# Optimization experiments

Hardware: AMD Instinct MI355X
Metric: run time of the kernel (lower is better)

## Reference

```python
import jax, jax.numpy as jnp
import numpy as np
import math

N_HEAD = 16
HEAD_DIM = 64
N_EMBD = 1024
EPS_RMS = 1e-5
U_L2_EPS = 1e-6

def _get_alibi_slopes(n_heads):
    def pow2(n):
        start = 2 ** (-2 ** (-(math.log2(n) - 3)))
        return [start * start ** i for i in range(n)]
    if math.log2(n_heads).is_integer():
        return pow2(n_heads)
    c = 2 ** math.floor(math.log2(n_heads))
    s = pow2(c)
    extra = _get_alibi_slopes(2 * c)
    return s + extra[0::2][: n_heads - c]

def setup_inputs() -> dict:
    key = jax.random.key(0)
    ks = jax.random.split(key, 9)
    B, T = 2, 2048
    H, D, C = N_HEAD, HEAD_DIM, N_EMBD
    x = jax.random.normal(ks[0], (B, T, C), dtype=jnp.float32)
    # Linear weights stored as [in, out] so y = x @ W
    sc = 1.0 / math.sqrt(C)
    Wq = jax.random.normal(ks[1], (C, H * D), dtype=jnp.float32) * sc
    Wk = jax.random.normal(ks[2], (C, H * D), dtype=jnp.float32) * sc
    Wv = jax.random.normal(ks[3], (C, H * D), dtype=jnp.float32) * sc
    Wproj = jax.random.normal(ks[4], (H * D, C), dtype=jnp.float32) * (0.5 / math.sqrt(C) / math.sqrt(12))
    q_rms_w = jnp.ones((D,), dtype=jnp.float32)
    k_rms_w = jnp.ones((D,), dtype=jnp.float32)
    # keygated bias params: omega init = softplus_inverse(1.0), u ~ N(0, 1/sqrt(D))
    omega = jnp.full((H,), math.log(math.expm1(1.0)), dtype=jnp.float32)
    u = jax.random.normal(ks[5], (H, D), dtype=jnp.float32) * (1.0 / math.sqrt(D))
    return {"x": x, "Wq": Wq, "Wk": Wk, "Wv": Wv, "Wproj": Wproj,
            "q_rms_w": q_rms_w, "k_rms_w": k_rms_w, "omega": omega, "u": u}

def _rmsnorm(x, w):
    var = jnp.mean(jnp.square(x), axis=-1, keepdims=True)
    return x * jax.lax.rsqrt(var + EPS_RMS) * w

def reference(x, Wq, Wk, Wv, Wproj, q_rms_w, k_rms_w, omega, u):
    B, T, C = x.shape
    H, D = N_HEAD, HEAD_DIM
    q = (x @ Wq).reshape(B, T, H, D)
    k = (x @ Wk).reshape(B, T, H, D)
    v = (x @ Wv).reshape(B, T, H, D)
    q = _rmsnorm(q, q_rms_w)
    k = _rmsnorm(k, k_rms_w)
    # key-gated additive bias
    slopes = jnp.asarray(_get_alibi_slopes(H), dtype=jnp.float32)  # [H]
    omega_eff = jax.nn.softplus(omega) * slopes                    # [H]
    u_n = u / jnp.maximum(jnp.linalg.norm(u, axis=-1, keepdims=True), U_L2_EPS)
    gate_logits = jnp.einsum('bthd,hd->bht', k, u_n) / math.sqrt(D)  # fp32
    gate = jax.nn.softplus(gate_logits)                            # [B,H,T]
    idx = jnp.arange(T)
    dist = jnp.maximum(idx[:, None] - idx[None, :], 0).astype(jnp.float32)  # [T,T]
    bias = -dist[None, None] * omega_eff[None, :, None, None] * gate[:, :, None, :]  # [B,H,T,T]
    causal = idx[:, None] >= idx[None, :]
    bias = jnp.where(causal[None, None], bias, -jnp.inf)
    # attention
    scale = 1.0 / math.sqrt(D)
    scores = jnp.einsum('bihd,bjhd->bhij', q, k) * scale + bias
    attn = jax.nn.softmax(scores, axis=-1)
    y = jnp.einsum('bhij,bjhd->bihd', attn, v).reshape(B, T, H * D)
    return y @ Wproj
```

## Files before the change

kernel.cpp:

```cpp
#include <hip/hip_runtime.h>
#include <hip/hip_bf16.h>

#define NH 16
#define HD 64
#define CE 1024
#define TT 2048
#define BB 2
#define MR (BB*TT)

typedef __attribute__((ext_vector_type(4))) float f32x4;
typedef __attribute__((ext_vector_type(8))) short s16x8;

__device__ __forceinline__ unsigned short f2b(float f) {
  union { __hip_bfloat16 b; unsigned short u; } t;
  t.b = __float2bfloat16(f);
  return t.u;
}
__device__ __forceinline__ float red64_sum(float v) {
#pragma unroll
  for (int m = 1; m < 64; m <<= 1) v += __shfl_xor(v, m, 64);
  return v;
}
__device__ __forceinline__ float red16_sum(float v) {
#pragma unroll
  for (int m = 1; m < 16; m <<= 1) v += __shfl_xor(v, m, 64);
  return v;
}
__device__ __forceinline__ float red16_max(float v) {
#pragma unroll
  for (int m = 1; m < 16; m <<= 1) v = fmaxf(v, __shfl_xor(v, m, 64));
  return v;
}
__device__ __forceinline__ float softplusf(float x) {
  return x > 20.0f ? x : log1pf(expf(x));
}

__global__ __launch_bounds__(256) void cvt_x(const float* __restrict__ x,
                                             unsigned short* __restrict__ xb, int n4) {
  int stride = gridDim.x * blockDim.x;
  for (int i = blockIdx.x * blockDim.x + threadIdx.x; i < n4; i += stride) {
    float4 v = ((const float4*)x)[i];
    union { unsigned short u[4]; uint2 p; } o;
    o.u[0] = f2b(v.x); o.u[1] = f2b(v.y); o.u[2] = f2b(v.z); o.u[3] = f2b(v.w);
    ((uint2*)xb)[i] = o.p;
  }
}

__global__ __launch_bounds__(256) void cvt_wt(const float* __restrict__ W0, const float* __restrict__ W1,
                                              const float* __restrict__ W2, const float* __restrict__ W3,
                                              unsigned short* __restrict__ T0, unsigned short* __restrict__ T1,
                                              unsigned short* __restrict__ T2, unsigned short* __restrict__ T3) {
  const float* W = blockIdx.z == 0 ? W0 : blockIdx.z == 1 ? W1 : blockIdx.z == 2 ? W2 : W3;
  unsigned short* T = blockIdx.z == 0 ? T0 : blockIdx.z == 1 ? T1 : blockIdx.z == 2 ? T2 : T3;
  __shared__ float t[64][65];
  int k0 = blockIdx.x * 64, n0 = blockIdx.y * 64;
  int row = threadIdx.x >> 2, seg = threadIdx.x & 3;
#pragma unroll
  for (int i = 0; i < 4; ++i) {
    float4 v = *(const float4*)(W + (size_t)(k0 + row) * CE + n0 + seg * 16 + i * 4);
    int c = seg * 16 + i * 4;
    t[row][c + 0] = v.x; t[row][c + 1] = v.y; t[row][c + 2] = v.z; t[row][c + 3] = v.w;
  }
  __syncthreads();
#pragma unroll
  for (int it = 0; it < 2; ++it) {
    int c = threadIdx.x + it * 256;
    int n = c >> 3, ks = (c & 7) * 8;
    union { unsigned short u[8]; uint4 p; } o;
#pragma unroll
    for (int e = 0; e < 8; ++e) o.u[e] = f2b(t[ks + e][n]);
    *(uint4*)(T + (size_t)(n0 + n) * CE + k0 + ks) = o.p;
  }
}

#define BM 128
#define BN 128
#define BK 64
__global__ __launch_bounds__(256) void gemm3(const unsigned short* __restrict__ A,
    const unsigned short* __restrict__ B0, const unsigned short* __restrict__ B1,
    const unsigned short* __restrict__ B2,
    float* __restrict__ C0, float* __restrict__ C1, float* __restrict__ C2,
    int M, int N, int K) {
  const unsigned short* Bt = blockIdx.z == 0 ? B0 : blockIdx.z == 1 ? B1 : B2;
  float* C = blockIdx.z == 0 ? C0 : blockIdx.z == 1 ? C1 : C2;
  __shared__ __align__(16) unsigned short aT[BM * BK];
  __shared__ __align__(16) unsigned short bT[BN * BK];
  int tid = threadIdx.x;
  int w = tid >> 6, lane = tid & 63, q4 = lane >> 4, r16 = lane & 15;
  int m0 = blockIdx.y * BM, n0 = blockIdx.x * BN;
  int wm = (w >> 1) * 64, wn = (w & 1) * 64;
  f32x4 acc[4][4] = {};
  for (int k0 = 0; k0 < K; k0 += BK) {
#pragma unroll
    for (int it = 0; it < 4; ++it) {
      int c = tid + it * 256;
      int row = c >> 3, sl = c & 7;
      s16x8 va = *(const s16x8*)(A + (size_t)(m0 + row) * K + k0 + sl * 8);
      *(s16x8*)((char*)aT + row * 128 + ((sl ^ (row & 7)) << 4)) = va;
      s16x8 vb = *(const s16x8*)(Bt + (size_t)(n0 + row) * K + k0 + sl * 8);
      *(s16x8*)((char*)bT + row * 128 + ((sl ^ (row & 7)) << 4)) = vb;
    }
    __syncthreads();
#pragma unroll
    for (int kk = 0; kk < 2; ++kk) {
      s16x8 af[4], bfr[4];
#pragma unroll
      for (int i = 0; i < 4; ++i) {
        int ra = wm + i * 16 + r16;
        af[i] = *(const s16x8*)((char*)aT + ra * 128 + ((((kk << 2) | q4) ^ (ra & 7)) << 4));
        int rb = wn + i * 16 + r16;
        bfr[i] = *(const s16x8*)((char*)bT + rb * 128 + ((((kk << 2) | q4) ^ (rb & 7)) << 4));
      }
#pragma unroll
      for (int i = 0; i < 4; ++i)
#pragma unroll
        for (int j = 0; j < 4; ++j)
          acc[i][j] = __builtin_amdgcn_mfma_f32_16x16x32_bf16(af[i], bfr[j], acc[i][j], 0, 0, 0);
    }
    __syncthreads();
  }
#pragma unroll
  for (int i = 0; i < 4; ++i)
#pragma unroll
    for (int j = 0; j < 4; ++j)
#pragma unroll
      for (int r = 0; r < 4; ++r) {
        int gm = m0 + wm + i * 16 + (q4 << 2) + r;
        int gn = n0 + wn + j * 16 + r16;
        C[(size_t)gm * N + gn] = acc[i][j][r];
      }
}

__global__ __launch_bounds__(256) void rmsgate(const float* __restrict__ q, const float* __restrict__ k,
    const float* __restrict__ v, const float* __restrict__ qw, const float* __restrict__ kw,
    const float* __restrict__ omega, const float* __restrict__ u,
    unsigned short* __restrict__ qb, unsigned short* __restrict__ kb,
    unsigned short* __restrict__ vtb, float* __restrict__ cg) {
  int b = blockIdx.z, h = blockIdx.y, t0 = blockIdx.x * 64;
  int tid = threadIdx.x, w = tid >> 6, lane = tid & 63;
  float uv = u[h * HD + lane];
  float us = red64_sum(uv * uv);
  float un = uv / fmaxf(sqrtf(us), 1e-6f);
  float qwl = qw[lane], kwl = kw[lane];
  float weff = softplusf(omega[h]) * exp2f(-0.5f * (float)(h + 1));
  size_t hb = ((size_t)(b * NH + h)) * TT;
#pragma unroll 4
  for (int it = 0; it < 16; ++it) {
    int t = t0 + w * 16 + it;
    size_t roff = ((size_t)(b * TT + t)) * CE + h * HD + lane;
    float qv = q[roff];
    float rq = rsqrtf(red64_sum(qv * qv) * (1.0f / 64.0f) + 1e-5f);
    qb[(hb + t) * HD + lane] = f2b(qv * rq * qwl * 0.125f);
    float kv = k[roff];
    float rk = rsqrtf(red64_sum(kv * kv) * (1.0f / 64.0f) + 1e-5f);
    float kn = kv * rk * kwl;
    kb[(hb + t) * HD + lane] = f2b(kn);
    float gl = red64_sum(kn * un) * 0.125f;
    if (lane == 0) cg[hb + t] = weff * softplusf(gl);
  }
  __shared__ unsigned short vt[64 * 65];
  int row = tid >> 2, seg = tid & 3;
#pragma unroll
  for (int i = 0; i < 4; ++i) {
    float4 vv = *(const float4*)(v + ((size_t)(b * TT + t0 + row)) * CE + h * HD + seg * 16 + i * 4);
    int d = seg * 16 + i * 4;
    vt[(d + 0) * 65 + row] = f2b(vv.x);
    vt[(d + 1) * 65 + row] = f2b(vv.y);
    vt[(d + 2) * 65 + row] = f2b(vv.z);
    vt[(d + 3) * 65 + row] = f2b(vv.w);
  }
  __syncthreads();
#pragma unroll
  for (int it = 0; it < 2; ++it) {
    int c = tid + it * 256;
    int d = c >> 3, js = (c & 7) * 8;
    union { unsigned short u[8]; uint4 p; } o;
#pragma unroll
    for (int e = 0; e < 8; ++e) o.u[e] = vt[d * 65 + js + e];
    *(uint4*)(vtb + (((size_t)(b * NH + h)) * HD + d) * TT + t0 + js) = o.p;
  }
}

#define QB 64
#define KVB 64
__global__ __launch_bounds__(256) void attn(const unsigned short* __restrict__ qb,
    const unsigned short* __restrict__ kb, const unsigned short* __restrict__ vtb,
    const float* __restrict__ cg, unsigned short* __restrict__ y) {
  int b = blockIdx.z, h = blockIdx.y, qt = blockIdx.x * QB;
  int tid = threadIdx.x, w = tid >> 6, lane = tid & 63, q4 = lane >> 4, r16 = lane & 15;
  __shared__ __align__(16) unsigned short kl[KVB * 64];
  __shared__ __align__(16) unsigned short vl[64 * KVB];
  __shared__ float cgl[KVB];
  __shared__ __align__(16) unsigned short pl[4][16 * 64];
  size_t hb = ((size_t)(b * NH + h)) * TT;
  int qrow = qt + w * 16 + r16;
  s16x8 qf[2];
  qf[0] = *(const s16x8*)(qb + (hb + qrow) * HD + q4 * 8);
  qf[1] = *(const s16x8*)(qb + (hb + qrow) * HD + 32 + q4 * 8);
  f32x4 acc[4] = {};
  float mr[4] = {-1e30f, -1e30f, -1e30f, -1e30f};
  float lr[4] = {0.f, 0.f, 0.f, 0.f};
  int i_base = qt + w * 16 + (q4 << 2);
  int nt = qt / KVB + 1;
  for (int jt = 0; jt < nt; ++jt) {
    int j0 = jt * KVB;
#pragma unroll
    for (int it = 0; it < 2; ++it) {
      int c = tid + (it << 8);
      int row = c >> 3, sl = c & 7;
      s16x8 kv8 = *(const s16x8*)(kb + (hb + j0 + row) * HD + sl * 8);
      *(s16x8*)((char*)kl + row * 128 + ((sl ^ (row & 7)) << 4)) = kv8;
      s16x8 vv8 = *(const s16x8*)(vtb + (((size_t)(b * NH + h)) * HD + row) * TT + j0 + sl * 8);
      *(s16x8*)((char*)vl + row * 128 + ((sl ^ (row & 7)) << 4)) = vv8;
    }
    if (tid < KVB) cgl[tid] = cg[hb + j0 + tid];
    __syncthreads();
    f32x4 s[4];
#pragma unroll
    for (int nf = 0; nf < 4; ++nf) {
      f32x4 z = {0.f, 0.f, 0.f, 0.f};
      int jr = nf * 16 + r16;
      s16x8 kf0 = *(const s16x8*)((char*)kl + jr * 128 + ((q4 ^ (jr & 7)) << 4));
      s16x8 kf1 = *(const s16x8*)((char*)kl + jr * 128 + (((4 | q4) ^ (jr & 7)) << 4));
      z = __builtin_amdgcn_mfma_f32_16x16x32_bf16(qf[0], kf0, z, 0, 0, 0);
      z = __builtin_amdgcn_mfma_f32_16x16x32_bf16(qf[1], kf1, z, 0, 0, 0);
      s[nf] = z;
    }
    float pmax[4] = {-1e30f, -1e30f, -1e30f, -1e30f};
#pragma unroll
    for (int nf = 0; nf < 4; ++nf) {
      int j = j0 + nf * 16 + r16;
      float cgj = cgl[nf * 16 + r16];
#pragma unroll
      for (int r = 0; r < 4; ++r) {
        int i = i_base + r;
        float sv = s[nf][r];
        sv = (j <= i) ? sv - (float)(i - j) * cgj : -1e30f;
        s[nf][r] = sv;
        pmax[r] = fmaxf(pmax[r], sv);
      }
    }
#pragma unroll
    for (int r = 0; r < 4; ++r) pmax[r] = red16_max(pmax[r]);
    float al[4], psum[4];
#pragma unroll
    for (int r = 0; r < 4; ++r) {
      float mn = fmaxf(mr[r], pmax[r]);
      al[r] = __expf(mr[r] - mn);
      mr[r] = mn;
      psum[r] = 0.f;
    }
#pragma unroll
    for (int nf = 0; nf < 4; ++nf) {
#pragma unroll
      for (int r = 0; r < 4; ++r) {
        float p = __expf(s[nf][r] - mr[r]);
        psum[r] += p;
        int il = (q4 << 2) + r;
        int slot = (((nf << 1) | (r16 >> 3)) ^ (il & 7));
        *(unsigned short*)((char*)pl[w] + il * 128 + (slot << 4) + ((r16 & 7) << 1)) = f2b(p);
      }
    }
#pragma unroll
    for (int r = 0; r < 4; ++r) {
      psum[r] = red16_sum(psum[r]);
      lr[r] = lr[r] * al[r] + psum[r];
    }
#pragma unroll
    for (int nf = 0; nf < 4; ++nf) {
      f32x4 a = acc[nf];
      a[0] *= al[0]; a[1] *= al[1]; a[2] *= al[2]; a[3] *= al[3];
      acc[nf] = a;
    }
    __syncthreads();
    s16x8 pa0 = *(const s16x8*)((char*)pl[w] + r16 * 128 + ((q4 ^ (r16 & 7)) << 4));
    s16x8 pa1 = *(const s16x8*)((char*)pl[w] + r16 * 128 + (((4 | q4) ^ (r16 & 7)) << 4));
#pragma unroll
    for (int nf = 0; nf < 4; ++nf) {
      int dr = nf * 16 + r16;
      s16x8 vf0 = *(const s16x8*)((char*)vl + dr * 128 + ((q4 ^ (dr & 7)) << 4));
      s16x8 vf1 = *(const s16x8*)((char*)vl + dr * 128 + (((4 | q4) ^ (dr & 7)) << 4));
      acc[nf] = __builtin_amdgcn_mfma_f32_16x16x32_bf16(pa0, vf0, acc[nf], 0, 0, 0);
      acc[nf] = __builtin_amdgcn_mfma_f32_16x16x32_bf16(pa1, vf1, acc[nf], 0, 0, 0);
    }
    __syncthreads();
  }
#pragma unroll
  for (int r = 0; r < 4; ++r) {
    float inv = 1.0f / lr[r];
    int i = i_base + r;
#pragma unroll
    for (int nf = 0; nf < 4; ++nf) {
      y[((size_t)(b * TT) + i) * CE + h * HD + nf * 16 + r16] = f2b(acc[nf][r] * inv);
    }
  }
}

extern "C" void kernel_launch(void* const* d_in, const int* in_sizes, int n_in,
                              void* d_out, int out_size, void* d_ws, size_t ws_size,
                              hipStream_t stream) {
  const float* x  = (const float*)d_in[0];
  const float* Wq = (const float*)d_in[1];
  const float* Wk = (const float*)d_in[2];
  const float* Wv = (const float*)d_in[3];
  const float* Wp = (const float*)d_in[4];
  const float* qw = (const float*)d_in[5];
  const float* kw = (const float*)d_in[6];
  const float* om = (const float*)d_in[7];
  const float* u  = (const float*)d_in[8];
  float* out = (float*)d_out;
  char* ws = (char*)d_ws;
  const size_t MB = 1024 * 1024;
  unsigned short* xb  = (unsigned short*)(ws + 0);
  unsigned short* wqt = (unsigned short*)(ws + 8 * MB);
  unsigned short* wkt = (unsigned short*)(ws + 10 * MB);
  unsigned short* wvt = (unsigned short*)(ws + 12 * MB);
  unsigned short* wpt = (unsigned short*)(ws + 14 * MB);
  float* qf = (float*)(ws + 16 * MB);
  float* kf = (float*)(ws + 32 * MB);
  float* vf = (float*)(ws + 48 * MB);
  unsigned short* qbb = (unsigned short*)(ws + 64 * MB);
  unsigned short* kbb = (unsigned short*)(ws + 72 * MB);
  unsigned short* vtb = (unsigned short*)(ws + 80 * MB);
  float* cg = (float*)(ws + 88 * MB);
  unsigned short* yb = (unsigned short*)(ws + 16 * MB);

  cvt_x<<<dim3(2048), dim3(256), 0, stream>>>(x, xb, MR * CE / 4);
  cvt_wt<<<dim3(16, 16, 4), dim3(256), 0, stream>>>(Wq, Wk, Wv, Wp, wqt, wkt, wvt, wpt);
  gemm3<<<dim3(8, 32, 3), dim3(256), 0, stream>>>(xb, wqt, wkt, wvt, qf, kf, vf, MR, CE, CE);
  rmsgate<<<dim3(32, 16, 2), dim3(256), 0, stream>>>(qf, kf, vf, qw, kw, om, u, qbb, kbb, vtb, cg);
  attn<<<dim3(32, 16, 2), dim3(256), 0, stream>>>(qbb, kbb, vtb, cg, yb);
  gemm3<<<dim3(8, 32, 1), dim3(256), 0, stream>>>(yb, wpt, wpt, wpt, out, out, out, MR, CE, CE);
}
```

Before: 322.0 us.

## Rework attention with 32x32 MFMA, register-resident P, and direct global-to-LDS loads

```diff
diff --git a/kernel.cpp b/kernel.cpp
--- a/kernel.cpp
+++ b/kernel.cpp
@@ -7,40 +7,41 @@
 #define TT 2048
 #define BB 2
 #define MR (BB*TT)
+#define SWZ(r) ((((r) & 7)) ^ (((r) >> 3) & 3))
 
 typedef __attribute__((ext_vector_type(4))) float f32x4;
+typedef __attribute__((ext_vector_type(16))) float f32x16;
 typedef __attribute__((ext_vector_type(8))) short s16x8;
-
-__device__ __forceinline__ unsigned short f2b(float f) {
-  union { __hip_bfloat16 b; unsigned short u; } t;
+typedef unsigned int u32;
+typedef unsigned short u16;
+
+__device__ __forceinline__ void gld16(const void* g, void* l) {
+  __builtin_amdgcn_global_load_lds((const __attribute__((address_space(1))) unsigned int*)g,
+                                   (__attribute__((address_space(3))) unsigned int*)l, 16, 0, 0);
+}
+__device__ __forceinline__ u16 f2b(float f) {
+  union { __hip_bfloat16 b; u16 u; } t;
   t.b = __float2bfloat16(f);
   return t.u;
 }
+__device__ __forceinline__ u32 pk2(float a, float b) {
+  return (u32)f2b(a) | ((u32)f2b(b) << 16);
+}
 __device__ __forceinline__ float red64_sum(float v) {
 #pragma unroll
   for (int m = 1; m < 64; m <<= 1) v += __shfl_xor(v, m, 64);
   return v;
 }
-__device__ __forceinline__ float red16_sum(float v) {
-#pragma unroll
-  for (int m = 1; m < 16; m <<= 1) v += __shfl_xor(v, m, 64);
-  return v;
-}
-__device__ __forceinline__ float red16_max(float v) {
-#pragma unroll
-  for (int m = 1; m < 16; m <<= 1) v = fmaxf(v, __shfl_xor(v, m, 64));
-  return v;
-}
 __device__ __forceinline__ float softplusf(float x) {
   return x > 20.0f ? x : log1pf(expf(x));
 }
 
 __global__ __launch_bounds__(256) void cvt_x(const float* __restrict__ x,
-                                             unsigned short* __restrict__ xb, int n4) {
+                                             u16* __restrict__ xb, int n4) {
   int stride = gridDim.x * blockDim.x;
   for (int i = blockIdx.x * blockDim.x + threadIdx.x; i < n4; i += stride) {
     float4 v = ((const float4*)x)[i];
-    union { unsigned short u[4]; uint2 p; } o;
+    union { u16 u[4]; uint2 p; } o;
     o.u[0] = f2b(v.x); o.u[1] = f2b(v.y); o.u[2] = f2b(v.z); o.u[3] = f2b(v.w);
     ((uint2*)xb)[i] = o.p;
   }
@@ -48,10 +49,10 @@
 
 __global__ __launch_bounds__(256) void cvt_wt(const float* __restrict__ W0, const float* __restrict__ W1,
                                               const float* __restrict__ W2, const float* __restrict__ W3,
-                                              unsigned short* __restrict__ T0, unsigned short* __restrict__ T1,
-                                              unsigned short* __restrict__ T2, unsigned short* __restrict__ T3) {
+                                              u16* __restrict__ T0, u16* __restrict__ T1,
+                                              u16* __restrict__ T2, u16* __restrict__ T3) {
   const float* W = blockIdx.z == 0 ? W0 : blockIdx.z == 1 ? W1 : blockIdx.z == 2 ? W2 : W3;
-  unsigned short* T = blockIdx.z == 0 ? T0 : blockIdx.z == 1 ? T1 : blockIdx.z == 2 ? T2 : T3;
+  u16* T = blockIdx.z == 0 ? T0 : blockIdx.z == 1 ? T1 : blockIdx.z == 2 ? T2 : T3;
   __shared__ float t[64][65];
   int k0 = blockIdx.x * 64, n0 = blockIdx.y * 64;
   int row = threadIdx.x >> 2, seg = threadIdx.x & 3;
@@ -66,7 +67,7 @@
   for (int it = 0; it < 2; ++it) {
     int c = threadIdx.x + it * 256;
     int n = c >> 3, ks = (c & 7) * 8;
-    union { unsigned short u[8]; uint4 p; } o;
+    union { u16 u[8]; uint4 p; } o;
 #pragma unroll
     for (int e = 0; e < 8; ++e) o.u[e] = f2b(t[ks + e][n]);
     *(uint4*)(T + (size_t)(n0 + n) * CE + k0 + ks) = o.p;
@@ -76,15 +77,15 @@
 #define BM 128
 #define BN 128
 #define BK 64
-__global__ __launch_bounds__(256) void gemm3(const unsigned short* __restrict__ A,
-    const unsigned short* __restrict__ B0, const unsigned short* __restrict__ B1,
-    const unsigned short* __restrict__ B2,
+__global__ __launch_bounds__(256) void gemm3(const u16* __restrict__ A,
+    const u16* __restrict__ B0, const u16* __restrict__ B1,
+    const u16* __restrict__ B2,
     float* __restrict__ C0, float* __restrict__ C1, float* __restrict__ C2,
     int M, int N, int K) {
-  const unsigned short* Bt = blockIdx.z == 0 ? B0 : blockIdx.z == 1 ? B1 : B2;
+  const u16* Bt = blockIdx.z == 0 ? B0 : blockIdx.z == 1 ? B1 : B2;
   float* C = blockIdx.z == 0 ? C0 : blockIdx.z == 1 ? C1 : C2;
-  __shared__ __align__(16) unsigned short aT[BM * BK];
-  __shared__ __align__(16) unsigned short bT[BN * BK];
+  __shared__ __align__(16) u16 aT[BM * BK];
+  __shared__ __align__(16) u16 bT[BN * BK];
   int tid = threadIdx.x;
   int w = tid >> 6, lane = tid & 63, q4 = lane >> 4, r16 = lane & 15;
   int m0 = blockIdx.y * BM, n0 = blockIdx.x * BN;
@@ -95,10 +96,8 @@
     for (int it = 0; it < 4; ++it) {
       int c = tid + it * 256;
       int row = c >> 3, sl = c & 7;
-      s16x8 va = *(const s16x8*)(A + (size_t)(m0 + row) * K + k0 + sl * 8);
-      *(s16x8*)((char*)aT + row * 128 + ((sl ^ (row & 7)) << 4)) = va;
-      s16x8 vb = *(const s16x8*)(Bt + (size_t)(n0 + row) * K + k0 + sl * 8);
-      *(s16x8*)((char*)bT + row * 128 + ((sl ^ (row & 7)) << 4)) = vb;
+      gld16(A + (size_t)(m0 + row) * K + k0 + ((sl ^ SWZ(row)) << 3), &aT[c * 8]);
+      gld16(Bt + (size_t)(n0 + row) * K + k0 + ((sl ^ SWZ(row)) << 3), &bT[c * 8]);
     }
     __syncthreads();
 #pragma unroll
@@ -107,9 +106,9 @@
 #pragma unroll
       for (int i = 0; i < 4; ++i) {
         int ra = wm + i * 16 + r16;
-        af[i] = *(const s16x8*)((char*)aT + ra * 128 + ((((kk << 2) | q4) ^ (ra & 7)) << 4));
+        af[i] = *(const s16x8*)((char*)aT + ra * 128 + ((((kk << 2) | q4) ^ SWZ(ra)) << 4));
         int rb = wn + i * 16 + r16;
-        bfr[i] = *(const s16x8*)((char*)bT + rb * 128 + ((((kk << 2) | q4) ^ (rb & 7)) << 4));
+        bfr[i] = *(const s16x8*)((char*)bT + rb * 128 + ((((kk << 2) | q4) ^ SWZ(rb)) << 4));
       }
 #pragma unroll
       for (int i = 0; i < 4; ++i)
@@ -134,8 +133,8 @@
 __global__ __launch_bounds__(256) void rmsgate(const float* __restrict__ q, const float* __restrict__ k,
     const float* __restrict__ v, const float* __restrict__ qw, const float* __restrict__ kw,
     const float* __restrict__ omega, const float* __restrict__ u,
-    unsigned short* __restrict__ qb, unsigned short* __restrict__ kb,
-    unsigned short* __restrict__ vtb, float* __restrict__ cg) {
+    u16* __restrict__ qb, u16* __restrict__ kb,
+    u16* __restrict__ vtb, float* __restrict__ cg) {
   int b = blockIdx.z, h = blockIdx.y, t0 = blockIdx.x * 64;
   int tid = threadIdx.x, w = tid >> 6, lane = tid & 63;
   float uv = u[h * HD + lane];
@@ -158,7 +157,7 @@
     float gl = red64_sum(kn * un) * 0.125f;
     if (lane == 0) cg[hb + t] = weff * softplusf(gl);
   }
-  __shared__ unsigned short vt[64 * 65];
+  __shared__ u16 vt[64 * 65];
   int row = tid >> 2, seg = tid & 3;
 #pragma unroll
   for (int i = 0; i < 4; ++i) {
@@ -174,125 +173,128 @@
   for (int it = 0; it < 2; ++it) {
     int c = tid + it * 256;
     int d = c >> 3, js = (c & 7) * 8;
-    union { unsigned short u[8]; uint4 p; } o;
+    union { u16 u[8]; uint4 p; } o;
 #pragma unroll
     for (int e = 0; e < 8; ++e) o.u[e] = vt[d * 65 + js + e];
     *(uint4*)(vtb + (((size_t)(b * NH + h)) * HD + d) * TT + t0 + js) = o.p;
   }
 }
 
-#define QB 64
 #define KVB 64
-__global__ __launch_bounds__(256) void attn(const unsigned short* __restrict__ qb,
-    const unsigned short* __restrict__ kb, const unsigned short* __restrict__ vtb,
-    const float* __restrict__ cg, unsigned short* __restrict__ y) {
-  int b = blockIdx.z, h = blockIdx.y, qt = blockIdx.x * QB;
-  int tid = threadIdx.x, w = tid >> 6, lane = tid & 63, q4 = lane >> 4, r16 = lane & 15;
-  __shared__ __align__(16) unsigned short kl[KVB * 64];
-  __shared__ __align__(16) unsigned short vl[64 * KVB];
+__global__ __launch_bounds__(256) void attn(const u16* __restrict__ qb,
+    const u16* __restrict__ kb, const u16* __restrict__ vtb,
+    const float* __restrict__ cg, u16* __restrict__ y) {
+  int b = blockIdx.z, h = blockIdx.y, qb0 = blockIdx.x * 128;
+  int tid = threadIdx.x, w = tid >> 6, lane = tid & 63;
+  int hi = lane >> 5, q5 = lane & 31;
+  __shared__ __align__(16) u16 kl[64 * 64];
+  __shared__ __align__(16) u16 vl[64 * 64];
   __shared__ float cgl[KVB];
-  __shared__ __align__(16) unsigned short pl[4][16 * 64];
   size_t hb = ((size_t)(b * NH + h)) * TT;
-  int qrow = qt + w * 16 + r16;
-  s16x8 qf[2];
-  qf[0] = *(const s16x8*)(qb + (hb + qrow) * HD + q4 * 8);
-  qf[1] = *(const s16x8*)(qb + (hb + qrow) * HD + 32 + q4 * 8);
-  f32x4 acc[4] = {};
-  float mr[4] = {-1e30f, -1e30f, -1e30f, -1e30f};
-  float lr[4] = {0.f, 0.f, 0.f, 0.f};
-  int i_base = qt + w * 16 + (q4 << 2);
-  int nt = qt / KVB + 1;
+  size_t vbase = ((size_t)(b * NH + h)) * HD;
+  int qrow = qb0 + w * 32 + q5;
+  s16x8 qf[4];
+#pragma unroll
+  for (int kc = 0; kc < 4; ++kc)
+    qf[kc] = *(const s16x8*)(qb + (hb + qrow) * HD + kc * 16 + hi * 8);
+  f32x16 accO[2] = {};
+  float m = -1e30f, l = 0.f;
+  int qhi = qb0 + w * 32 + 31;
+  int nt = (qb0 + 128) / KVB;
   for (int jt = 0; jt < nt; ++jt) {
     int j0 = jt * KVB;
 #pragma unroll
     for (int it = 0; it < 2; ++it) {
       int c = tid + (it << 8);
       int row = c >> 3, sl = c & 7;
-      s16x8 kv8 = *(const s16x8*)(kb + (hb + j0 + row) * HD + sl * 8);
-      *(s16x8*)((char*)kl + row * 128 + ((sl ^ (row & 7)) << 4)) = kv8;
-      s16x8 vv8 = *(const s16x8*)(vtb + (((size_t)(b * NH + h)) * HD + row) * TT + j0 + sl * 8);
-      *(s16x8*)((char*)vl + row * 128 + ((sl ^ (row & 7)) << 4)) = vv8;
+      gld16(kb + (hb + j0 + row) * HD + ((sl ^ SWZ(row)) << 3), &kl[c * 8]);
+      gld16(vtb + (vbase + row) * TT + j0 + ((sl ^ SWZ(row)) << 3), &vl[c * 8]);
     }
     if (tid < KVB) cgl[tid] = cg[hb + j0 + tid];
     __syncthreads();
-    f32x4 s[4];
-#pragma unroll
-    for (int nf = 0; nf < 4; ++nf) {
-      f32x4 z = {0.f, 0.f, 0.f, 0.f};
-      int jr = nf * 16 + r16;
-      s16x8 kf0 = *(const s16x8*)((char*)kl + jr * 128 + ((q4 ^ (jr & 7)) << 4));
-      s16x8 kf1 = *(const s16x8*)((char*)kl + jr * 128 + (((4 | q4) ^ (jr & 7)) << 4));
-      z = __builtin_amdgcn_mfma_f32_16x16x32_bf16(qf[0], kf0, z, 0, 0, 0);
-      z = __builtin_amdgcn_mfma_f32_16x16x32_bf16(qf[1], kf1, z, 0, 0, 0);
-      s[nf] = z;
-    }
-    float pmax[4] = {-1e30f, -1e30f, -1e30f, -1e30f};
-#pragma unroll
-    for (int nf = 0; nf < 4; ++nf) {
-      int j = j0 + nf * 16 + r16;
-      float cgj = cgl[nf * 16 + r16];
-#pragma unroll
-      for (int r = 0; r < 4; ++r) {
-        int i = i_base + r;
-        float sv = s[nf][r];
-        sv = (j <= i) ? sv - (float)(i - j) * cgj : -1e30f;
-        s[nf][r] = sv;
-        pmax[r] = fmaxf(pmax[r], sv);
-      }
-    }
-#pragma unroll
-    for (int r = 0; r < 4; ++r) pmax[r] = red16_max(pmax[r]);
-    float al[4], psum[4];
-#pragma unroll
-    for (int r = 0; r < 4; ++r) {
-      float mn = fmaxf(mr[r], pmax[r]);
-      al[r] = __expf(mr[r] - mn);
-      mr[r] = mn;
-      psum[r] = 0.f;
-    }
-#pragma unroll
-    for (int nf = 0; nf < 4; ++nf) {
-#pragma unroll
-      for (int r = 0; r < 4; ++r) {
-        float p = __expf(s[nf][r] - mr[r]);
-        psum[r] += p;
-        int il = (q4 << 2) + r;
-        int slot = (((nf << 1) | (r16 >> 3)) ^ (il & 7));
-        *(unsigned short*)((char*)pl[w] + il * 128 + (slot << 4) + ((r16 & 7) << 1)) = f2b(p);
-      }
-    }
-#pragma unroll
-    for (int r = 0; r < 4; ++r) {
-      psum[r] = red16_sum(psum[r]);
-      lr[r] = lr[r] * al[r] + psum[r];
-    }
-#pragma unroll
-    for (int nf = 0; nf < 4; ++nf) {
-      f32x4 a = acc[nf];
-      a[0] *= al[0]; a[1] *= al[1]; a[2] *= al[2]; a[3] *= al[3];
-      acc[nf] = a;
+    if (j0 <= qhi) {
+      f32x16 s0 = {}, s1 = {};
+#pragma unroll
+      for (int kc = 0; kc < 4; ++kc) {
+        int r0 = q5;
+        s16x8 kf0 = *(const s16x8*)((char*)kl + r0 * 128 + ((((kc << 1) | hi) ^ SWZ(r0)) << 4));
+        s0 = __builtin_amdgcn_mfma_f32_32x32x16_bf16(kf0, qf[kc], s0, 0, 0, 0);
+        int r1 = q5 + 32;
+        s16x8 kf1 = *(const s16x8*)((char*)kl + r1 * 128 + ((((kc << 1) | hi) ^ SWZ(r1)) << 4));
+        s1 = __builtin_amdgcn_mfma_f32_32x32x16_bf16(kf1, qf[kc], s1, 0, 0, 0);
+      }
+      float pmax = -1e30f;
+#pragma unroll
+      for (int r = 0; r < 16; ++r) {
+        int kvl = (r & 3) + 8 * (r >> 2) + 4 * hi;
+        int j = j0 + kvl;
+        float sv = s0[r];
+        sv = (j <= qrow) ? sv - (float)(qrow - j) * cgl[kvl] : -1e30f;
+        s0[r] = sv; pmax = fmaxf(pmax, sv);
+        int j2 = j0 + 32 + kvl;
+        float sv1 = s1[r];
+        sv1 = (j2 <= qrow) ? sv1 - (float)(qrow - j2) * cgl[32 + kvl] : -1e30f;
+        s1[r] = sv1; pmax = fmaxf(pmax, sv1);
+      }
+      pmax = fmaxf(pmax, __shfl_xor(pmax, 32, 64));
+      float mn = fmaxf(m, pmax);
+      float al = __expf(m - mn);
+      m = mn;
+      float ps = 0.f;
+#pragma unroll
+      for (int r = 0; r < 16; ++r) {
+        float p0 = __expf(s0[r] - m); s0[r] = p0;
+        float p1 = __expf(s1[r] - m); s1[r] = p1;
+        ps += p0 + p1;
+      }
+      ps += __shfl_xor(ps, 32, 64);
+      l = l * al + ps;
+#pragma unroll
+      for (int r = 0; r < 16; ++r) { accO[0][r] *= al; accO[1][r] *= al; }
+      auto pvchunk = [&](f32x16 sc, int cb4) {
+        u32 c01 = pk2(sc[0], sc[1]),  c23 = pk2(sc[2], sc[3]);
+        u32 c45 = pk2(sc[4], sc[5]),  c67 = pk2(sc[6], sc[7]);
+        u32 c89 = pk2(sc[8], sc[9]),  cAB = pk2(sc[10], sc[11]);
+        u32 cCD = pk2(sc[12], sc[13]), cEF = pk2(sc[14], sc[15]);
+        u32 x01 = (u32)__shfl_xor((int)c01, 32, 64), x23 = (u32)__shfl_xor((int)c23, 32, 64);
+        u32 x45 = (u32)__shfl_xor((int)c45, 32, 64), x67 = (u32)__shfl_xor((int)c67, 32, 64);
+        u32 x89 = (u32)__shfl_xor((int)c89, 32, 64), xAB = (u32)__shfl_xor((int)cAB, 32, 64);
+        u32 xCD = (u32)__shfl_xor((int)cCD, 32, 64), xEF = (u32)__shfl_xor((int)cEF, 32, 64);
+        union { u32 wd[4]; s16x8 v; } Bf0, Bf1;
+        Bf0.wd[0] = hi ? x45 : c01; Bf0.wd[1] = hi ? x67 : c23;
+        Bf0.wd[2] = hi ? c45 : x01; Bf0.wd[3] = hi ? c67 : x23;
+        Bf1.wd[0] = hi ? xCD : c89; Bf1.wd[1] = hi ? xEF : cAB;
+        Bf1.wd[2] = hi ? cCD : x89; Bf1.wd[3] = hi ? cEF : xAB;
+#pragma unroll
+        for (int dt = 0; dt < 2; ++dt) {
+          int dr = q5 + 32 * dt;
+          s16x8 vf0 = *(const s16x8*)((char*)vl + dr * 128 + (((cb4 | hi) ^ SWZ(dr)) << 4));
+          s16x8 vf1 = *(const s16x8*)((char*)vl + dr * 128 + ((((cb4 | 2) | hi) ^ SWZ(dr)) << 4));
+          accO[dt] = __builtin_amdgcn_mfma_f32_32x32x16_bf16(vf0, Bf0.v, accO[dt], 0, 0, 0);
+          accO[dt] = __builtin_amdgcn_mfma_f32_32x32x16_bf16(vf1, Bf1.v, accO[dt], 0, 0, 0);
+        }
+      };
+      pvchunk(s0, 0);
+      pvchunk(s1, 4);
     }
     __syncthreads();
-    s16x8 pa0 = *(const s16x8*)((char*)pl[w] + r16 * 128 + ((q4 ^ (r16 & 7)) << 4));
-    s16x8 pa1 = *(const s16x8*)((char*)pl[w] + r16 * 128 + (((4 | q4) ^ (r16 & 7)) << 4));
-#pragma unroll
-    for (int nf = 0; nf < 4; ++nf) {
-      int dr = nf * 16 + r16;
-      s16x8 vf0 = *(const s16x8*)((char*)vl + dr * 128 + ((q4 ^ (dr & 7)) << 4));
-      s16x8 vf1 = *(const s16x8*)((char*)vl + dr * 128 + (((4 | q4) ^ (dr & 7)) << 4));
-      acc[nf] = __builtin_amdgcn_mfma_f32_16x16x32_bf16(pa0, vf0, acc[nf], 0, 0, 0);
-      acc[nf] = __builtin_amdgcn_mfma_f32_16x16x32_bf16(pa1, vf1, acc[nf], 0, 0, 0);
-    }
-    __syncthreads();
-  }
-#pragma unroll
-  for (int r = 0; r < 4; ++r) {
-    float inv = 1.0f / lr[r];
-    int i = i_base + r;
-#pragma unroll
-    for (int nf = 0; nf < 4; ++nf) {
-      y[((size_t)(b * TT) + i) * CE + h * HD + nf * 16 + r16] = f2b(acc[nf][r] * inv);
-    }
+  }
+  u16* obase = (w < 2) ? (kl + w * 2048) : (vl + (w - 2) * 2048);
+  float inv = 1.f / l;
+#pragma unroll
+  for (int dt = 0; dt < 2; ++dt)
+#pragma unroll
+    for (int r = 0; r < 16; ++r) {
+      int d = 32 * dt + (r & 3) + 8 * (r >> 2) + 4 * hi;
+      *(u16*)((char*)obase + q5 * 128 + ((((d >> 3)) ^ SWZ(q5)) << 4) + ((d & 7) << 1)) = f2b(accO[dt][r] * inv);
+    }
+  __syncthreads();
+  int row = lane >> 1, half = lane & 1;
+#pragma unroll
+  for (int s4 = 0; s4 < 4; ++s4) {
+    int slot = half * 4 + s4;
+    s16x8 vv = *(const s16x8*)((char*)obase + row * 128 + ((slot ^ SWZ(row)) << 4));
+    *(s16x8*)(y + ((size_t)(b * TT) + qb0 + w * 32 + row) * CE + h * HD + half * 32 + s4 * 8) = vv;
   }
 }
 
@@ -311,24 +313,24 @@
   float* out = (float*)d_out;
   char* ws = (char*)d_ws;
   const size_t MB = 1024 * 1024;
-  unsigned short* xb  = (unsigned short*)(ws + 0);
-  unsigned short* wqt = (unsigned short*)(ws + 8 * MB);
-  unsigned short* wkt = (unsigned short*)(ws + 10 * MB);
-  unsigned short* wvt = (unsigned short*)(ws + 12 * MB);
-  unsigned short* wpt = (unsigned short*)(ws + 14 * MB);
+  u16* xb  = (u16*)(ws + 0);
+  u16* wqt = (u16*)(ws + 8 * MB);
+  u16* wkt = (u16*)(ws + 10 * MB);
+  u16* wvt = (u16*)(ws + 12 * MB);
+  u16* wpt = (u16*)(ws + 14 * MB);
   float* qf = (float*)(ws + 16 * MB);
   float* kf = (float*)(ws + 32 * MB);
   float* vf = (float*)(ws + 48 * MB);
-  unsigned short* qbb = (unsigned short*)(ws + 64 * MB);
-  unsigned short* kbb = (unsigned short*)(ws + 72 * MB);
-  unsigned short* vtb = (unsigned short*)(ws + 80 * MB);
+  u16* qbb = (u16*)(ws + 64 * MB);
+  u16* kbb = (u16*)(ws + 72 * MB);
+  u16* vtb = (u16*)(ws + 80 * MB);
   float* cg = (float*)(ws + 88 * MB);
-  unsigned short* yb = (unsigned short*)(ws + 16 * MB);
+  u16* yb = (u16*)(ws + 16 * MB);
 
   cvt_x<<<dim3(2048), dim3(256), 0, stream>>>(x, xb, MR * CE / 4);
   cvt_wt<<<dim3(16, 16, 4), dim3(256), 0, stream>>>(Wq, Wk, Wv, Wp, wqt, wkt, wvt, wpt);
   gemm3<<<dim3(8, 32, 3), dim3(256), 0, stream>>>(xb, wqt, wkt, wvt, qf, kf, vf, MR, CE, CE);
   rmsgate<<<dim3(32, 16, 2), dim3(256), 0, stream>>>(qf, kf, vf, qw, kw, om, u, qbb, kbb, vtb, cg);
-  attn<<<dim3(32, 16, 2), dim3(256), 0, stream>>>(qbb, kbb, vtb, cg, yb);
+  attn<<<dim3(16, 16, 2), dim3(256), 0, stream>>>(qbb, kbb, vtb, cg, yb);
   gemm3<<<dim3(8, 32, 1), dim3(256), 0, stream>>>(yb, wpt, wpt, wpt, out, out, out, MR, CE, CE);
 }
```

Measured after the change: 307.3 us. 4.6% less time.
